# Kernel tuning notes

Measured on AMD Instinct MI355X. Metric: run time of the kernel, lower is better.

## Reference

```python
import jax, jax.numpy as jnp
import numpy as np

EPS = 1e-5
GROUPS = 8


def _bn(x, gamma, beta, mean, var, axis):
    # inference-mode batchnorm along `axis`
    shape = [1] * x.ndim
    shape[axis] = -1
    scale = gamma.reshape(shape) * jax.lax.rsqrt(var.reshape(shape) + EPS)
    return (x - mean.reshape(shape)) * scale + beta.reshape(shape)


def setup_inputs() -> dict:
    key = jax.random.key(0)
    ks = jax.random.split(key, 16)
    N, C, H, W = 8, 128, 128, 128
    out_planes = 128
    x = jax.random.normal(ks[0], (N, C, H, W), jnp.float32)
    w_qkv = jax.random.normal(ks[1], (2 * out_planes, C), jnp.float32) * np.float32(np.sqrt(1.0 / C))

    def bn_params(k, c):
        k1, k2, k3, k4 = jax.random.split(k, 4)
        gamma = jax.random.uniform(k1, (c,), jnp.float32, 0.5, 1.5)
        beta = jax.random.normal(k2, (c,), jnp.float32) * 0.1
        mean = jax.random.normal(k3, (c,), jnp.float32) * 0.1
        var = jax.random.uniform(k4, (c,), jnp.float32, 0.5, 1.5)
        return gamma, beta, mean, var

    qg, qb, qm, qv = bn_params(ks[2], 2 * out_planes)
    sg, sb, sm, sv = bn_params(ks[3], GROUPS)
    og, ob, om, ov = bn_params(ks[4], out_planes)
    return {
        'x': x, 'w_qkv': w_qkv,
        'qkv_gamma': qg, 'qkv_beta': qb, 'qkv_mean': qm, 'qkv_var': qv,
        'sim_gamma': sg, 'sim_beta': sb, 'sim_mean': sm, 'sim_var': sv,
        'out_gamma': og, 'out_beta': ob, 'out_mean': om, 'out_var': ov,
    }


def reference(x, w_qkv, qkv_gamma, qkv_beta, qkv_mean, qkv_var,
              sim_gamma, sim_beta, sim_mean, sim_var,
              out_gamma, out_beta, out_mean, out_var):
    N, C, H, W = x.shape
    groups = GROUPS
    out_planes = w_qkv.shape[0] // 2
    gp = out_planes // groups  # group_planes

    # width=False: (N,C,H,W) -> (N,W,C,H) -> (N*W, C, H)
    xb = jnp.transpose(x, (0, 3, 1, 2)).reshape(N * W, C, H)
    # conv1x1 qkv transform + BN1d over channels
    qkv = jnp.einsum('bci,oc->boi', xb, w_qkv)
    qkv = _bn(qkv, qkv_gamma, qkv_beta, qkv_mean, qkv_var, axis=1)
    qkv = qkv.reshape(N * W, groups, 2 * gp, H)
    q = qkv[:, :, : gp // 2]          # (NW, g, gp/2, H)
    k = qkv[:, :, gp // 2: gp]        # (NW, g, gp/2, H)
    v = qkv[:, :, gp:]                # (NW, g, gp,   H)

    qk = jnp.einsum('bgci,bgcj->bgij', q, k)  # (NW, g, H, H)
    sim = _bn(qk, sim_gamma, sim_beta, sim_mean, sim_var, axis=1)
    sim = jax.nn.softmax(sim, axis=3)

    sv = jnp.einsum('bgij,bgcj->bgci', sim, v)  # (NW, g, gp, H)
    sv = sv.reshape(N * W, out_planes, H)
    out = _bn(sv, out_gamma, out_beta, out_mean, out_var, axis=1)
    out = out.reshape(N, W, out_planes, H)
    # permute(0,2,3,1): (N, out_planes, H, W)
    return jnp.transpose(out, (0, 2, 3, 1))
```

## Files before the change

kernel.cpp:

```cpp
#include <hip/hip_runtime.h>
#include <math.h>

#define EPS 1e-5f

typedef _Float16 half4 __attribute__((ext_vector_type(4)));
typedef _Float16 half8 __attribute__((ext_vector_type(8)));
typedef float floatx4 __attribute__((ext_vector_type(4)));

__global__ void transpose_cvt_k(const float* __restrict__ x, _Float16* __restrict__ xt2) {
  __shared__ float tile[64][65];
  int nh = blockIdx.x;
  int n = nh >> 7, h = nh & 127;
  int c0 = blockIdx.y * 64, w0 = blockIdx.z * 64;
  const float* src = x + (size_t)n * 2097152 + (size_t)h * 128;
  _Float16* dst = xt2 + (size_t)n * 2097152 + (size_t)h * 128;
  int lane = threadIdx.x & 63;
  int tr = threadIdx.x >> 6;
#pragma unroll
  for (int rr = tr; rr < 64; rr += 4)
    tile[rr][lane] = src[(size_t)(c0 + rr) * 16384 + w0 + lane];
  __syncthreads();
#pragma unroll
  for (int cc = tr; cc < 64; cc += 4)
    dst[(size_t)(w0 + cc) * 16384 + c0 + lane] = (_Float16)tile[lane][cc];
}

__global__ void __launch_bounds__(256, 2) qkv_mfma_kernel(
    const _Float16* __restrict__ xt2, const float* __restrict__ wq,
    const float* __restrict__ qg, const float* __restrict__ qb,
    const float* __restrict__ qm, const float* __restrict__ qv,
    _Float16* __restrict__ qkv16) {
  __shared__ _Float16 As[128][136];
  __shared__ _Float16 Bs[128][136];
  __shared__ float scs[128];
  __shared__ float bis[128];
  int b = blockIdx.x >> 1;
  int oh = blockIdx.x & 1;
  int t = threadIdx.x;

  {
    const float* wbase = wq + (size_t)oh * 128 * 128;
#pragma unroll
    for (int idx = t; idx < 4096; idx += 256) {
      int o = idx >> 5, c4 = (idx & 31) * 4;
      float4 v = *(const float4*)(wbase + (size_t)o * 128 + c4);
      half4 hv;
      hv[0] = (_Float16)v.x;
      hv[1] = (_Float16)v.y;
      hv[2] = (_Float16)v.z;
      hv[3] = (_Float16)v.w;
      *(half4*)(&As[o][c4]) = hv;
    }
  }
  {
    const _Float16* xb = xt2 + (size_t)b * 16384;
#pragma unroll
    for (int idx = t; idx < 2048; idx += 256) {
      int i = idx >> 4, c8 = (idx & 15) * 8;
      half8 v = *(const half8*)(xb + (size_t)i * 128 + c8);
      *(half8*)(&Bs[i][c8]) = v;
    }
  }
  if (t < 128) {
    int o = oh * 128 + t;
    float sc = qg[o] * rsqrtf(qv[o] + EPS);
    scs[t] = sc;
    bis[t] = qb[o] - qm[o] * sc;
  }
  __syncthreads();

  int wv = t >> 6;
  int lane = t & 63;
  int m0 = (wv & 1) * 64;
  int n0 = (wv >> 1) * 64;
  int lrow = lane & 15;
  int quad = lane >> 4;

  floatx4 acc[4][4];
#pragma unroll
  for (int mt = 0; mt < 4; mt++)
#pragma unroll
    for (int nt = 0; nt < 4; nt++)
#pragma unroll
      for (int r = 0; r < 4; r++) acc[mt][nt][r] = 0.f;

#pragma unroll
  for (int k0 = 0; k0 < 128; k0 += 32) {
    half8 af[4], bf[4];
#pragma unroll
    for (int mt = 0; mt < 4; mt++)
      af[mt] = *(const half8*)(&As[m0 + mt * 16 + lrow][k0 + quad * 8]);
#pragma unroll
    for (int nt = 0; nt < 4; nt++)
      bf[nt] = *(const half8*)(&Bs[n0 + nt * 16 + lrow][k0 + quad * 8]);
#pragma unroll
    for (int mt = 0; mt < 4; mt++)
#pragma unroll
      for (int nt = 0; nt < 4; nt++)
        acc[mt][nt] = __builtin_amdgcn_mfma_f32_16x16x32_f16(af[mt], bf[nt], acc[mt][nt], 0, 0, 0);
  }

  _Float16* outb = qkv16 + (size_t)b * 32768 + (size_t)oh * 16384;
#pragma unroll
  for (int mt = 0; mt < 4; mt++) {
#pragma unroll
    for (int r = 0; r < 4; r++) {
      int o_l = m0 + mt * 16 + quad * 4 + r;
      float sc = scs[o_l];
      float bi = bis[o_l];
#pragma unroll
      for (int nt = 0; nt < 4; nt++) {
        int i = n0 + nt * 16 + lrow;
        outb[(size_t)o_l * 128 + i] = (_Float16)fmaf(acc[mt][nt][r], sc, bi);
      }
    }
  }
}

__global__ void __launch_bounds__(512, 4) attn_mfma_fused_kernel(
    const _Float16* __restrict__ qkv16,
    const float* __restrict__ sg, const float* __restrict__ sb,
    const float* __restrict__ sm, const float* __restrict__ svv,
    const float* __restrict__ og, const float* __restrict__ obt,
    const float* __restrict__ om, const float* __restrict__ ov,
    float* __restrict__ out) {
  __shared__ _Float16 olds[16][128][8];
  __shared__ _Float16 plds[8][2176];
  int bid = blockIdx.x;
  int nn = bid >> 7;
  int g = (bid >> 4) & 7;
  int wt = bid & 15;
  int t = threadIdx.x;
  int wv = t >> 6;
  int lane = t & 63;
  int ln = lane & 15;
  int q4 = lane >> 4;

  float s_scale = sg[g] * rsqrtf(svv[g] + EPS);
  float sc4 = s_scale * 0.25f * 1.44269504f;
  (void)sb;
  (void)sm;

  float osc[4], obi[4];
#pragma unroll
  for (int r = 0; r < 4; r++) {
    int oc = g * 16 + q4 * 4 + r;
    float s0 = og[oc] * rsqrtf(ov[oc] + EPS);
    osc[r] = s0;
    obi[r] = obt[oc] - om[oc] * s0;
  }

  _Float16* pw = &plds[wv][0];
  int b = nn * 128 + wt * 8 + wv;
  const _Float16* base = qkv16 + (size_t)b * 32768 + (size_t)g * 4096;
  const _Float16* kb = base + 1024;
  const _Float16* vb = base + 2048;

  half8 kf[8];
#pragma unroll
  for (int jt = 0; jt < 8; jt++)
#pragma unroll
    for (int jj = 0; jj < 8; jj++)
      kf[jt][jj] = kb[jj * 128 + jt * 16 + ln];

  half8 vf[4];
#pragma unroll
  for (int ks = 0; ks < 4; ks++)
    vf[ks] = *(const half8*)(vb + (size_t)ln * 128 + ks * 32 + q4 * 8);

  for (int st8 = 0; st8 < 8; st8++) {
    half8 qf;
#pragma unroll
    for (int jj = 0; jj < 8; jj++)
      qf[jj] = base[jj * 128 + st8 * 16 + ln];

    floatx4 stt[8];
#pragma unroll
    for (int jt = 0; jt < 8; jt++) {
      floatx4 z = {0.f, 0.f, 0.f, 0.f};
      stt[jt] = __builtin_amdgcn_mfma_f32_16x16x32_f16(kf[jt], qf, z, 0, 0, 0);
    }

    float mx = -1e30f;
#pragma unroll
    for (int jt = 0; jt < 8; jt++)
#pragma unroll
      for (int r = 0; r < 4; r++) {
        stt[jt][r] *= sc4;
        mx = fmaxf(mx, stt[jt][r]);
      }
    mx = fmaxf(mx, __shfl_xor(mx, 16));
    mx = fmaxf(mx, __shfl_xor(mx, 32));

    float ls = 0.f;
#pragma unroll
    for (int jt = 0; jt < 8; jt++)
#pragma unroll
      for (int r = 0; r < 4; r++) {
        float e = exp2f(stt[jt][r] - mx);
        stt[jt][r] = e;
        ls += e;
      }
    ls += __shfl_xor(ls, 16);
    ls += __shfl_xor(ls, 32);

#pragma unroll
    for (int jt = 0; jt < 8; jt++) {
      half4 h;
      h[0] = (_Float16)stt[jt][0];
      h[1] = (_Float16)stt[jt][1];
      h[2] = (_Float16)stt[jt][2];
      h[3] = (_Float16)stt[jt][3];
      *(half4*)(&pw[ln * 136 + jt * 16 + q4 * 4]) = h;
    }

    floatx4 oacc = {0.f, 0.f, 0.f, 0.f};
#pragma unroll
    for (int ks = 0; ks < 4; ks++) {
      half8 pf = *(const half8*)(&pw[ln * 136 + ks * 32 + q4 * 8]);
      oacc = __builtin_amdgcn_mfma_f32_16x16x32_f16(vf[ks], pf, oacc, 0, 0, 0);
    }

    float invl = 1.f / ls;
#pragma unroll
    for (int r = 0; r < 4; r++)
      olds[q4 * 4 + r][st8 * 16 + ln][wv] = (_Float16)fmaf(oacc[r] * invl, osc[r], obi[r]);
  }

  __syncthreads();

  float* outp = out + ((size_t)nn * 128 + g * 16) * 16384 + wt * 8;
#pragma unroll
  for (int idx = t; idx < 4096; idx += 512) {
    int w4 = idx & 1;
    int h = (idx >> 1) & 127;
    int c = idx >> 8;
    half4 v = *(const half4*)(&olds[c][h][w4 * 4]);
    float4 f;
    f.x = (float)v[0];
    f.y = (float)v[1];
    f.z = (float)v[2];
    f.w = (float)v[3];
    *(float4*)(outp + (size_t)c * 16384 + (size_t)h * 128 + w4 * 4) = f;
  }
}

extern "C" void kernel_launch(void* const* d_in, const int* in_sizes, int n_in,
                              void* d_out, int out_size, void* d_ws, size_t ws_size,
                              hipStream_t stream) {
  const float* x  = (const float*)d_in[0];
  const float* wq = (const float*)d_in[1];
  const float* qg = (const float*)d_in[2];
  const float* qb = (const float*)d_in[3];
  const float* qm = (const float*)d_in[4];
  const float* qv = (const float*)d_in[5];
  const float* sg = (const float*)d_in[6];
  const float* sb = (const float*)d_in[7];
  const float* sm = (const float*)d_in[8];
  const float* sv = (const float*)d_in[9];
  const float* og = (const float*)d_in[10];
  const float* ob = (const float*)d_in[11];
  const float* om = (const float*)d_in[12];
  const float* ov = (const float*)d_in[13];
  float* out = (float*)d_out;

  _Float16* qkv16 = (_Float16*)d_ws;
  _Float16* xt2 = qkv16 + (size_t)1024 * 256 * 128;

  transpose_cvt_k<<<dim3(1024, 2, 2), 256, 0, stream>>>(x, xt2);
  qkv_mfma_kernel<<<2048, 256, 0, stream>>>(xt2, wq, qg, qb, qm, qv, qkv16);
  attn_mfma_fused_kernel<<<1024, 512, 0, stream>>>(qkv16, sg, sb, sm, sv,
                                                   og, ob, om, ov, out);
}
```

Measured before the change: 262.3 us.

## Fold BN scales into fp16 weights, compute softmax sum via MFMA, swizzle output LDS

Precomputes fp16 weights with the qkv BN scale and the similarity BN/softmax scale folded into the q rows. This lets the qkv GEMM read operands straight from global memory without LDS staging and add only a bias. The attention kernel drops the per-element scale and computes the row sum with an MFMA against a ones vector. It splits the P tile into two halves to shrink LDS, uses a fast reciprocal, exp and packed conversions, and XOR-swizzles the output LDS buffer. Occupancy hints are raised. Folding the scale into fp16 weights and dropping LDS reuse in the GEMM may affect precision and memory traffic.

```diff
diff --git a/kernel.cpp b/kernel.cpp
--- a/kernel.cpp
+++ b/kernel.cpp
@@ -3,11 +3,65 @@
 
 #define EPS 1e-5f
 
+typedef _Float16 half2t __attribute__((ext_vector_type(2)));
 typedef _Float16 half4 __attribute__((ext_vector_type(4)));
 typedef _Float16 half8 __attribute__((ext_vector_type(8)));
 typedef float floatx4 __attribute__((ext_vector_type(4)));
 
-__global__ void transpose_cvt_k(const float* __restrict__ x, _Float16* __restrict__ xt2) {
+#if __has_builtin(__builtin_amdgcn_exp2f)
+#define EXP2F __builtin_amdgcn_exp2f
+#else
+#define EXP2F exp2f
+#endif
+
+static __device__ __forceinline__ float fast_rcp(float x) {
+#if __has_builtin(__builtin_amdgcn_rcpf)
+  return __builtin_amdgcn_rcpf(x);
+#else
+  return 1.f / x;
+#endif
+}
+
+static __device__ __forceinline__ half4 pack4(float a, float b, float c, float d) {
+#if __has_builtin(__builtin_amdgcn_cvt_pkrtz)
+  auto lo = __builtin_amdgcn_cvt_pkrtz(a, b);
+  auto hi = __builtin_amdgcn_cvt_pkrtz(c, d);
+  half4 h;
+  h[0] = (_Float16)lo[0];
+  h[1] = (_Float16)lo[1];
+  h[2] = (_Float16)hi[0];
+  h[3] = (_Float16)hi[1];
+  return h;
+#else
+  half4 h;
+  h[0] = (_Float16)a; h[1] = (_Float16)b; h[2] = (_Float16)c; h[3] = (_Float16)d;
+  return h;
+#endif
+}
+
+__global__ void transpose_cvt_k(const float* __restrict__ x, _Float16* __restrict__ xt2,
+                                const float* __restrict__ wq,
+                                const float* __restrict__ qg, const float* __restrict__ qb,
+                                const float* __restrict__ qm, const float* __restrict__ qv,
+                                const float* __restrict__ sg, const float* __restrict__ svv,
+                                _Float16* __restrict__ w16, float* __restrict__ bis) {
+  if (blockIdx.y == 0 && blockIdx.z == 0 && blockIdx.x < 256) {
+    int tt = threadIdx.x;
+    int o = blockIdx.x;
+    if (tt < 128) {
+      int g = o >> 5, ch = o & 31;
+      float sc = qg[o] * rsqrtf(qv[o] + EPS);
+      float bi = qb[o] - qm[o] * sc;
+      if (ch < 8) {
+        float al = sg[g] * rsqrtf(svv[g] + EPS) * (0.25f * 1.44269504f);
+        sc *= al;
+        bi *= al;
+      }
+      w16[o * 128 + tt] = (_Float16)(wq[o * 128 + tt] * sc);
+      if (tt == 0) bis[o] = bi;
+    }
+  }
+
   __shared__ float tile[64][65];
   int nh = blockIdx.x;
   int n = nh >> 7, h = nh & 127;
@@ -25,56 +79,22 @@
     dst[(size_t)(w0 + cc) * 16384 + c0 + lane] = (_Float16)tile[lane][cc];
 }
 
-__global__ void __launch_bounds__(256, 2) qkv_mfma_kernel(
-    const _Float16* __restrict__ xt2, const float* __restrict__ wq,
-    const float* __restrict__ qg, const float* __restrict__ qb,
-    const float* __restrict__ qm, const float* __restrict__ qv,
-    _Float16* __restrict__ qkv16) {
-  __shared__ _Float16 As[128][136];
-  __shared__ _Float16 Bs[128][136];
-  __shared__ float scs[128];
-  __shared__ float bis[128];
-  int b = blockIdx.x >> 1;
-  int oh = blockIdx.x & 1;
+__global__ void __launch_bounds__(256, 4) qkv_mfma_kernel(
+    const _Float16* __restrict__ xt2, const _Float16* __restrict__ w16,
+    const float* __restrict__ bis, _Float16* __restrict__ qkv16) {
+  int bid = blockIdx.x;
+  int oh = bid >> 10;
+  int b = bid & 1023;
   int t = threadIdx.x;
-
-  {
-    const float* wbase = wq + (size_t)oh * 128 * 128;
-#pragma unroll
-    for (int idx = t; idx < 4096; idx += 256) {
-      int o = idx >> 5, c4 = (idx & 31) * 4;
-      float4 v = *(const float4*)(wbase + (size_t)o * 128 + c4);
-      half4 hv;
-      hv[0] = (_Float16)v.x;
-      hv[1] = (_Float16)v.y;
-      hv[2] = (_Float16)v.z;
-      hv[3] = (_Float16)v.w;
-      *(half4*)(&As[o][c4]) = hv;
-    }
-  }
-  {
-    const _Float16* xb = xt2 + (size_t)b * 16384;
-#pragma unroll
-    for (int idx = t; idx < 2048; idx += 256) {
-      int i = idx >> 4, c8 = (idx & 15) * 8;
-      half8 v = *(const half8*)(xb + (size_t)i * 128 + c8);
-      *(half8*)(&Bs[i][c8]) = v;
-    }
-  }
-  if (t < 128) {
-    int o = oh * 128 + t;
-    float sc = qg[o] * rsqrtf(qv[o] + EPS);
-    scs[t] = sc;
-    bis[t] = qb[o] - qm[o] * sc;
-  }
-  __syncthreads();
-
   int wv = t >> 6;
   int lane = t & 63;
   int m0 = (wv & 1) * 64;
   int n0 = (wv >> 1) * 64;
-  int lrow = lane & 15;
-  int quad = lane >> 4;
+  int ln = lane & 15;
+  int q4 = lane >> 4;
+
+  const _Float16* wb = w16 + (size_t)oh * 16384;
+  const _Float16* xb = xt2 + (size_t)b * 16384;
 
   floatx4 acc[4][4];
 #pragma unroll
@@ -89,10 +109,10 @@
     half8 af[4], bf[4];
 #pragma unroll
     for (int mt = 0; mt < 4; mt++)
-      af[mt] = *(const half8*)(&As[m0 + mt * 16 + lrow][k0 + quad * 8]);
+      af[mt] = *(const half8*)(wb + (size_t)(m0 + mt * 16 + ln) * 128 + k0 + q4 * 8);
 #pragma unroll
     for (int nt = 0; nt < 4; nt++)
-      bf[nt] = *(const half8*)(&Bs[n0 + nt * 16 + lrow][k0 + quad * 8]);
+      bf[nt] = *(const half8*)(xb + (size_t)(n0 + nt * 16 + ln) * 128 + k0 + q4 * 8);
 #pragma unroll
     for (int mt = 0; mt < 4; mt++)
 #pragma unroll
@@ -103,29 +123,27 @@
   _Float16* outb = qkv16 + (size_t)b * 32768 + (size_t)oh * 16384;
 #pragma unroll
   for (int mt = 0; mt < 4; mt++) {
+    float4 bi4 = *(const float4*)(bis + oh * 128 + m0 + mt * 16 + q4 * 4);
 #pragma unroll
     for (int r = 0; r < 4; r++) {
-      int o_l = m0 + mt * 16 + quad * 4 + r;
-      float sc = scs[o_l];
-      float bi = bis[o_l];
+      int o_l = m0 + mt * 16 + q4 * 4 + r;
+      float bi = (r == 0) ? bi4.x : (r == 1) ? bi4.y : (r == 2) ? bi4.z : bi4.w;
 #pragma unroll
       for (int nt = 0; nt < 4; nt++) {
-        int i = n0 + nt * 16 + lrow;
-        outb[(size_t)o_l * 128 + i] = (_Float16)fmaf(acc[mt][nt][r], sc, bi);
+        int i = n0 + nt * 16 + ln;
+        outb[(size_t)o_l * 128 + i] = (_Float16)(acc[mt][nt][r] + bi);
       }
     }
   }
 }
 
-__global__ void __launch_bounds__(512, 4) attn_mfma_fused_kernel(
+__global__ void __launch_bounds__(512, 6) attn_mfma_fused_kernel(
     const _Float16* __restrict__ qkv16,
-    const float* __restrict__ sg, const float* __restrict__ sb,
-    const float* __restrict__ sm, const float* __restrict__ svv,
     const float* __restrict__ og, const float* __restrict__ obt,
     const float* __restrict__ om, const float* __restrict__ ov,
     float* __restrict__ out) {
-  __shared__ _Float16 olds[16][128][8];
-  __shared__ _Float16 plds[8][2176];
+  __shared__ _Float16 olds[16384];
+  __shared__ _Float16 plds[8][1152];
   int bid = blockIdx.x;
   int nn = bid >> 7;
   int g = (bid >> 4) & 7;
@@ -136,11 +154,6 @@
   int ln = lane & 15;
   int q4 = lane >> 4;
 
-  float s_scale = sg[g] * rsqrtf(svv[g] + EPS);
-  float sc4 = s_scale * 0.25f * 1.44269504f;
-  (void)sb;
-  (void)sm;
-
   float osc[4], obi[4];
 #pragma unroll
   for (int r = 0; r < 4; r++) {
@@ -150,6 +163,10 @@
     obi[r] = obt[oc] - om[oc] * s0;
   }
 
+  half8 onesv;
+#pragma unroll
+  for (int i = 0; i < 8; i++) onesv[i] = (_Float16)1.0f;
+
   _Float16* pw = &plds[wv][0];
   int b = nn * 128 + wt * 8 + wv;
   const _Float16* base = qkv16 + (size_t)b * 32768 + (size_t)g * 4096;
@@ -181,50 +198,52 @@
       stt[jt] = __builtin_amdgcn_mfma_f32_16x16x32_f16(kf[jt], qf, z, 0, 0, 0);
     }
 
-    float mx = -1e30f;
-#pragma unroll
-    for (int jt = 0; jt < 8; jt++)
-#pragma unroll
-      for (int r = 0; r < 4; r++) {
-        stt[jt][r] *= sc4;
-        mx = fmaxf(mx, stt[jt][r]);
-      }
+    float mx = fmaxf(stt[0][0], stt[0][1]);
+    mx = fmaxf(fmaxf(mx, stt[0][2]), stt[0][3]);
+#pragma unroll
+    for (int jt = 1; jt < 8; jt++) {
+      mx = fmaxf(fmaxf(mx, stt[jt][0]), stt[jt][1]);
+      mx = fmaxf(fmaxf(mx, stt[jt][2]), stt[jt][3]);
+    }
     mx = fmaxf(mx, __shfl_xor(mx, 16));
     mx = fmaxf(mx, __shfl_xor(mx, 32));
 
-    float ls = 0.f;
-#pragma unroll
-    for (int jt = 0; jt < 8; jt++)
-#pragma unroll
-      for (int r = 0; r < 4; r++) {
-        float e = exp2f(stt[jt][r] - mx);
-        stt[jt][r] = e;
-        ls += e;
-      }
-    ls += __shfl_xor(ls, 16);
-    ls += __shfl_xor(ls, 32);
-
-#pragma unroll
-    for (int jt = 0; jt < 8; jt++) {
-      half4 h;
-      h[0] = (_Float16)stt[jt][0];
-      h[1] = (_Float16)stt[jt][1];
-      h[2] = (_Float16)stt[jt][2];
-      h[3] = (_Float16)stt[jt][3];
-      *(half4*)(&pw[ln * 136 + jt * 16 + q4 * 4]) = h;
-    }
-
     floatx4 oacc = {0.f, 0.f, 0.f, 0.f};
-#pragma unroll
-    for (int ks = 0; ks < 4; ks++) {
-      half8 pf = *(const half8*)(&pw[ln * 136 + ks * 32 + q4 * 8]);
+    floatx4 lacc = {0.f, 0.f, 0.f, 0.f};
+
+#pragma unroll
+    for (int jt = 0; jt < 4; jt++) {
+      half4 h = pack4(EXP2F(stt[jt][0] - mx), EXP2F(stt[jt][1] - mx),
+                      EXP2F(stt[jt][2] - mx), EXP2F(stt[jt][3] - mx));
+      *(half4*)(&pw[ln * 72 + jt * 16 + q4 * 4]) = h;
+    }
+#pragma unroll
+    for (int ks = 0; ks < 2; ks++) {
+      half8 pf = *(const half8*)(&pw[ln * 72 + ks * 32 + q4 * 8]);
       oacc = __builtin_amdgcn_mfma_f32_16x16x32_f16(vf[ks], pf, oacc, 0, 0, 0);
-    }
-
-    float invl = 1.f / ls;
-#pragma unroll
-    for (int r = 0; r < 4; r++)
-      olds[q4 * 4 + r][st8 * 16 + ln][wv] = (_Float16)fmaf(oacc[r] * invl, osc[r], obi[r]);
+      lacc = __builtin_amdgcn_mfma_f32_16x16x32_f16(onesv, pf, lacc, 0, 0, 0);
+    }
+#pragma unroll
+    for (int jt = 0; jt < 4; jt++) {
+      half4 h = pack4(EXP2F(stt[jt + 4][0] - mx), EXP2F(stt[jt + 4][1] - mx),
+                      EXP2F(stt[jt + 4][2] - mx), EXP2F(stt[jt + 4][3] - mx));
+      *(half4*)(&pw[ln * 72 + jt * 16 + q4 * 4]) = h;
+    }
+#pragma unroll
+    for (int ks = 0; ks < 2; ks++) {
+      half8 pf = *(const half8*)(&pw[ln * 72 + ks * 32 + q4 * 8]);
+      oacc = __builtin_amdgcn_mfma_f32_16x16x32_f16(vf[ks + 2], pf, oacc, 0, 0, 0);
+      lacc = __builtin_amdgcn_mfma_f32_16x16x32_f16(onesv, pf, lacc, 0, 0, 0);
+    }
+
+    float invl = fast_rcp(lacc[0]);
+#pragma unroll
+    for (int r = 0; r < 4; r++) {
+      int c = q4 * 4 + r;
+      int idx = (c << 10) + ((st8 * 16 + ln) << 3) + wv;
+      idx ^= (q4 & 3) << 2;
+      olds[idx] = (_Float16)fmaf(oacc[r] * invl, osc[r], obi[r]);
+    }
   }
 
   __syncthreads();
@@ -235,7 +254,9 @@
     int w4 = idx & 1;
     int h = (idx >> 1) & 127;
     int c = idx >> 8;
-    half4 v = *(const half4*)(&olds[c][h][w4 * 4]);
+    int hidx = (c << 10) + (h << 3) + w4 * 4;
+    hidx ^= ((c >> 2) & 3) << 2;
+    half4 v = *(const half4*)(&olds[hidx]);
     float4 f;
     f.x = (float)v[0];
     f.y = (float)v[1];
@@ -263,12 +284,16 @@
   const float* om = (const float*)d_in[12];
   const float* ov = (const float*)d_in[13];
   float* out = (float*)d_out;
+  (void)sb;
+  (void)sm;
 
   _Float16* qkv16 = (_Float16*)d_ws;
   _Float16* xt2 = qkv16 + (size_t)1024 * 256 * 128;
-
-  transpose_cvt_k<<<dim3(1024, 2, 2), 256, 0, stream>>>(x, xt2);
-  qkv_mfma_kernel<<<2048, 256, 0, stream>>>(xt2, wq, qg, qb, qm, qv, qkv16);
-  attn_mfma_fused_kernel<<<1024, 512, 0, stream>>>(qkv16, sg, sb, sm, sv,
-                                                   og, ob, om, ov, out);
-}
+  _Float16* w16 = xt2 + (size_t)1024 * 128 * 128;
+  float* bis = (float*)(w16 + 256 * 128);
+
+  transpose_cvt_k<<<dim3(1024, 2, 2), 256, 0, stream>>>(x, xt2, wq, qg, qb, qm, qv,
+                                                        sg, sv, w16, bis);
+  qkv_mfma_kernel<<<2048, 256, 0, stream>>>(xt2, w16, bis, qkv16);
+  attn_mfma_fused_kernel<<<1024, 512, 0, stream>>>(qkv16, og, ob, om, ov, out);
+}
```

Measured after the change: 323.4 us. 1.23x slower.
